# Performance work log

Measured on AMD Instinct MI355X. Metric: run time of the kernel, lower is better.

The kernel has to match this reference:

```python
import jax, jax.numpy as jnp
import numpy as np

SUB_NO = 5
T_NO = 201
H_NO = 64
T_DATA = 50000
E_SYN = 2000
I_SYN = 200


def setup_inputs() -> dict:
    key = jax.random.key(0)
    ks = jax.random.split(key, 10)
    k_conv = 1.0 / np.sqrt(2 * T_NO)   # pytorch Conv1d init bound: 1/sqrt(in_ch/groups * k)
    k_ff = 1.0 / np.sqrt(H_NO)
    k_root = 1.0 / np.sqrt(SUB_NO)
    return {
        "S_e": jax.random.uniform(ks[0], (T_DATA, E_SYN), dtype=jnp.float32),
        "S_i": jax.random.uniform(ks[1], (T_DATA, I_SYN), dtype=jnp.float32),
        "temp": jnp.ones((), dtype=jnp.float32),
        "C_syn_e_raw": jnp.ones((SUB_NO, E_SYN), dtype=jnp.float32),
        "C_syn_i_raw": jnp.ones((SUB_NO, I_SYN), dtype=jnp.float32),
        "conv_w": jax.random.uniform(ks[2], (H_NO * SUB_NO, 2, T_NO), jnp.float32, -k_conv, k_conv),
        "conv_b": jax.random.uniform(ks[3], (H_NO * SUB_NO,), jnp.float32, -k_conv, k_conv),
        "ff_w": jax.random.uniform(ks[4], (SUB_NO, H_NO), jnp.float32, -k_ff, k_ff),
        "ff_b": jax.random.uniform(ks[5], (SUB_NO,), jnp.float32, -k_ff, k_ff),
        "root_w": jax.random.uniform(ks[6], (SUB_NO,), jnp.float32, -k_root, k_root),
        "root_b": jax.random.uniform(ks[7], (), jnp.float32, -k_root, k_root),
        "V_o": jax.random.normal(ks[8], (1,), dtype=jnp.float32),
    }


def reference(S_e, S_i, temp, C_syn_e_raw, C_syn_i_raw, conv_w, conv_b,
              ff_w, ff_b, root_w, root_b, V_o):
    T_data = S_e.shape[0]
    # softmax over subunit axis (axis 0) of the synapse->subunit assignment logits
    C_syn_e = jax.nn.softmax(C_syn_e_raw / temp, axis=0)  # (sub, E)
    C_syn_i = jax.nn.softmax(C_syn_i_raw / temp, axis=0)  # (sub, I)
    S_e_group = S_e @ C_syn_e.T  # (T, sub)
    S_i_group = S_i @ C_syn_i.T  # (T, sub)
    # interleave: channel 2s = excit, 2s+1 = inhib  -> (T, 2*sub)
    S = jnp.stack([S_e_group, S_i_group], axis=2).reshape(T_data, 2 * SUB_NO)
    S = S.T[None]  # (1, 2*sub, T)
    conv_out = jax.lax.conv_general_dilated(
        S, conv_w,
        window_strides=(1,),
        padding=[(T_NO // 2, T_NO // 2)],
        feature_group_count=SUB_NO,
        dimension_numbers=("NCH", "OIH", "NCH"),
    ) + conv_b[None, :, None]          # (1, sub*H, T)
    conv_out = conv_out[0].reshape(SUB_NO, H_NO, T_data)  # (sub, H, T)
    # per-subunit Linear(H,1) + LeakyReLU, fused as an einsum
    sub_out = jnp.einsum("sht,sh->ts", conv_out, ff_w) + ff_b  # (T, sub)
    sub_out = jax.nn.leaky_relu(sub_out, 0.01)
    root_out = jax.nn.leaky_relu(sub_out @ root_w + root_b, 0.01) + V_o[0]  # (T,)
    return root_out
```

## Files before the change

### kernel.cpp

```cpp
#include <hip/hip_runtime.h>
#include <math.h>

#define SUB 5
#define TNO 201
#define HNO 64
#define TDATA 50000
#define ESYN 2000
#define ISYN 200
#define PAD (TNO/2)

#define QE (ESYN/4)
#define QI (ISYN/4)
#define CP 21
#define LDSC ((QE+QI)*CP)

__global__ void weff_kernel(const float* __restrict__ conv_w,
                            const float* __restrict__ conv_b,
                            const float* __restrict__ ff_w,
                            const float* __restrict__ ff_b,
                            float* __restrict__ Weff,
                            float* __restrict__ beff) {
    int idx = blockIdx.x * blockDim.x + threadIdx.x;
    if (idx < SUB * 2 * TNO) {
        int s   = idx / (2 * TNO);
        int rem = idx - s * (2 * TNO);
        float acc = 0.f;
        #pragma unroll 8
        for (int h = 0; h < HNO; ++h)
            acc = fmaf(ff_w[s * HNO + h], conv_w[(size_t)(s * HNO + h) * (2 * TNO) + rem], acc);
        Weff[idx] = acc;
    }
    if (idx < SUB) {
        float acc = ff_b[idx];
        for (int h = 0; h < HNO; ++h)
            acc = fmaf(ff_w[idx * HNO + h], conv_b[idx * HNO + h], acc);
        beff[idx] = acc;
    }
}

__device__ inline float elemf(float4 v, int e) {
    switch (e) { case 0: return v.x; case 1: return v.y; case 2: return v.z; default: return v.w; }
}

__device__ inline float foldp(float a, float b, int m, int lane) {
    float send = (lane & m) ? a : b;
    float recv = __shfl_xor(send, m);
    return ((lane & m) ? b : a) + recv;
}

template<int CH0>
__device__ inline void fma_block(float (&acc)[4][10],
                                 float4 v0, float4 v1, float4 v2, float4 v3,
                                 const float* c) {
    #pragma unroll
    for (int e = 0; e < 4; ++e) {
        float a0 = elemf(v0, e), a1 = elemf(v1, e), a2 = elemf(v2, e), a3 = elemf(v3, e);
        #pragma unroll
        for (int s = 0; s < 5; ++s) {
            float w = c[e * 5 + s];
            acc[0][2 * s + CH0] = fmaf(a0, w, acc[0][2 * s + CH0]);
            acc[1][2 * s + CH0] = fmaf(a1, w, acc[1][2 * s + CH0]);
            acc[2][2 * s + CH0] = fmaf(a2, w, acc[2][2 * s + CH0]);
            acc[3][2 * s + CH0] = fmaf(a3, w, acc[3][2 * s + CH0]);
        }
    }
}

__global__ __launch_bounds__(256) void group_kernel(
        const float* __restrict__ Se, const float* __restrict__ Si,
        const float* __restrict__ rawE, const float* __restrict__ rawI,
        const float* __restrict__ temp,
        float* __restrict__ Sg) {
    __shared__ float ldsC[LDSC];

    float invT = 1.0f / temp[0];
    for (int j = threadIdx.x; j < ESYN + ISYN; j += blockDim.x) {
        float v[SUB];
        float* dst;
        if (j < ESYN) {
            #pragma unroll
            for (int s = 0; s < SUB; ++s) v[s] = rawE[s * ESYN + j] * invT;
            dst = ldsC + (j >> 2) * CP + (j & 3) * SUB;
        } else {
            int jj = j - ESYN;
            #pragma unroll
            for (int s = 0; s < SUB; ++s) v[s] = rawI[s * ISYN + jj] * invT;
            dst = ldsC + QE * CP + (jj >> 2) * CP + (jj & 3) * SUB;
        }
        float m = fmaxf(fmaxf(fmaxf(v[0], v[1]), fmaxf(v[2], v[3])), v[4]);
        float sum = 0.f;
        #pragma unroll
        for (int s = 0; s < SUB; ++s) { v[s] = expf(v[s] - m); sum += v[s]; }
        float r = 1.0f / sum;
        #pragma unroll
        for (int s = 0; s < SUB; ++s) dst[s] = v[s] * r;
    }
    __syncthreads();

    const float* lE = ldsC;
    const float* lI = ldsC + QE * CP;
    int wave = threadIdx.x >> 6;
    int lane = threadIdx.x & 63;
    int nw   = (gridDim.x * blockDim.x) >> 6;
    int wid  = blockIdx.x * (blockDim.x >> 6) + wave;

    for (int g = wid; g < TDATA / 4; g += nw) {
        int t0 = g * 4;
        float acc[4][10];
        #pragma unroll
        for (int r = 0; r < 4; ++r)
            #pragma unroll
            for (int c = 0; c < 10; ++c) acc[r][c] = 0.f;

        const float4* R0 = (const float4*)(Se + (size_t)(t0 + 0) * ESYN);
        const float4* R1 = (const float4*)(Se + (size_t)(t0 + 1) * ESYN);
        const float4* R2 = (const float4*)(Se + (size_t)(t0 + 2) * ESYN);
        const float4* R3 = (const float4*)(Se + (size_t)(t0 + 3) * ESYN);

        for (int it = 0; it < 7; ++it) {
            int q = lane + (it << 6);
            float4 v0 = R0[q], v1 = R1[q], v2 = R2[q], v3 = R3[q];
            fma_block<0>(acc, v0, v1, v2, v3, lE + q * CP);
        }
        {
            int q = lane + 448;
            float4 z = make_float4(0.f, 0.f, 0.f, 0.f);
            float4 v0 = z, v1 = z, v2 = z, v3 = z;
            if (q < QE) { v0 = R0[q]; v1 = R1[q]; v2 = R2[q]; v3 = R3[q]; }
            int qc = (q < QE) ? q : 0;
            fma_block<0>(acc, v0, v1, v2, v3, lE + qc * CP);
        }
        if (lane < QI) {
            const float4* I0 = (const float4*)(Si + (size_t)(t0 + 0) * ISYN);
            const float4* I1 = (const float4*)(Si + (size_t)(t0 + 1) * ISYN);
            const float4* I2 = (const float4*)(Si + (size_t)(t0 + 2) * ISYN);
            const float4* I3 = (const float4*)(Si + (size_t)(t0 + 3) * ISYN);
            float4 v0 = I0[lane], v1 = I1[lane], v2 = I2[lane], v3 = I3[lane];
            fma_block<1>(acc, v0, v1, v2, v3, lI + lane * CP);
        }

        float f1[20], f2[10], f3[5];
        {
            const float* a = &acc[0][0];
            #pragma unroll
            for (int j = 0; j < 20; ++j) f1[j] = foldp(a[2 * j], a[2 * j + 1], 1, lane);
            #pragma unroll
            for (int j = 0; j < 10; ++j) f2[j] = foldp(f1[2 * j], f1[2 * j + 1], 2, lane);
            #pragma unroll
            for (int j = 0; j < 5; ++j)  f3[j] = foldp(f2[2 * j], f2[2 * j + 1], 4, lane);
            #pragma unroll
            for (int j = 0; j < 5; ++j) {
                f3[j] += __shfl_xor(f3[j], 8);
                f3[j] += __shfl_xor(f3[j], 16);
                f3[j] += __shfl_xor(f3[j], 32);
            }
        }
        if (lane < 8) {
            #pragma unroll
            for (int j = 0; j < 5; ++j) {
                int i = 8 * j + lane;
                int r = i / 10, c = i - 10 * r;
                Sg[(size_t)(t0 + r) * 10 + c] = f3[j];
            }
        }
    }
}

#define OB 128
#define ORS (OB + TNO - 1)

__global__ __launch_bounds__(128) void out_kernel(
        const float* __restrict__ Sg, const float* __restrict__ Weff,
        const float* __restrict__ beff, const float* __restrict__ root_w,
        const float* __restrict__ root_b, const float* __restrict__ V_o,
        float* __restrict__ out) {
    __shared__ float sS[ORS * 10];

    int tid = threadIdx.x;
    int t0  = blockIdx.x * OB;

    for (int i = tid; i < ORS * 5; i += OB) {
        int rr = i / 5, p = i - rr * 5;
        int rg = t0 - PAD + rr;
        float2 val = make_float2(0.f, 0.f);
        if (rg >= 0 && rg < TDATA) val = *(const float2*)(Sg + (size_t)rg * 10 + p * 2);
        *(float2*)(sS + rr * 10 + p * 2) = val;
    }
    __syncthreads();

    int t = t0 + tid;
    if (t >= TDATA) return;

    float acc[SUB];
    #pragma unroll
    for (int s = 0; s < SUB; ++s) acc[s] = beff[s];

    for (int k = 0; k < TNO; ++k) {
        const float* r = sS + (tid + k) * 10;
        #pragma unroll
        for (int s = 0; s < SUB; ++s) {
            float2 ei = *(const float2*)(r + 2 * s);
            acc[s] = fmaf(ei.x, Weff[s * 402 + k],
                     fmaf(ei.y, Weff[s * 402 + 201 + k], acc[s]));
        }
    }
    auto lk = [](float x) { return x > 0.f ? x : 0.01f * x; };
    float root = root_b[0];
    #pragma unroll
    for (int s = 0; s < SUB; ++s) root += lk(acc[s]) * root_w[s];
    out[t] = lk(root) + V_o[0];
}

extern "C" void kernel_launch(void* const* d_in, const int* in_sizes, int n_in,
                              void* d_out, int out_size, void* d_ws, size_t ws_size,
                              hipStream_t stream) {
    (void)in_sizes; (void)n_in; (void)out_size; (void)ws_size;
    const float* Se     = (const float*)d_in[0];
    const float* Si     = (const float*)d_in[1];
    const float* temp   = (const float*)d_in[2];
    const float* rawE   = (const float*)d_in[3];
    const float* rawI   = (const float*)d_in[4];
    const float* conv_w = (const float*)d_in[5];
    const float* conv_b = (const float*)d_in[6];
    const float* ff_w   = (const float*)d_in[7];
    const float* ff_b   = (const float*)d_in[8];
    const float* root_w = (const float*)d_in[9];
    const float* root_b = (const float*)d_in[10];
    const float* V_o    = (const float*)d_in[11];
    float* out = (float*)d_out;

    float* ws   = (float*)d_ws;
    float* Weff = ws;
    float* beff = ws + 2016;
    float* Sg   = ws + 2048;

    hipLaunchKernelGGL(weff_kernel, dim3(8), dim3(256), 0, stream,
                       conv_w, conv_b, ff_w, ff_b, Weff, beff);
    hipLaunchKernelGGL(group_kernel, dim3(768), dim3(256), 0, stream,
                       Se, Si, rawE, rawI, temp, Sg);
    hipLaunchKernelGGL(out_kernel, dim3((TDATA + OB - 1) / OB), dim3(128), 0, stream,
                       Sg, Weff, beff, root_w, root_b, V_o, out);
}
```

Baseline: 612.5 us.

## Software-pipeline Se loads with nontemporal prefetch and re-layout out_kernel LDS

Restructures the group kernel's row-tile loop so the next chunk of Se (and the first chunk of the next group) is loaded nontemporally while the current chunk is multiplied, and hoists the Si loads ahead of the FMA work. It also raises the launch-bounds occupancy hint to 3 blocks per CU. In out_kernel, the shared-memory staging is transposed to a per-subunit planar layout with padded pitch, and the tap loop gets partial unrolling, aiming to cut LDS bank conflicts. The prefetching raises register pressure, which may conflict with the occupancy target.

After: 716.0 us. +16.9%, slower.

```diff
diff --git a/kernel.cpp b/kernel.cpp
--- a/kernel.cpp
+++ b/kernel.cpp
@@ -13,6 +13,9 @@
 #define QI (ISYN/4)
 #define CP 21
 #define LDSC ((QE+QI)*CP)
+#define NGRP (TDATA/4)
+
+typedef float fx4 __attribute__((ext_vector_type(4)));
 
 __global__ void weff_kernel(const float* __restrict__ conv_w,
                             const float* __restrict__ conv_b,
@@ -38,10 +41,6 @@
     }
 }
 
-__device__ inline float elemf(float4 v, int e) {
-    switch (e) { case 0: return v.x; case 1: return v.y; case 2: return v.z; default: return v.w; }
-}
-
 __device__ inline float foldp(float a, float b, int m, int lane) {
     float send = (lane & m) ? a : b;
     float recv = __shfl_xor(send, m);
@@ -50,23 +49,22 @@
 
 template<int CH0>
 __device__ inline void fma_block(float (&acc)[4][10],
-                                 float4 v0, float4 v1, float4 v2, float4 v3,
+                                 fx4 v0, fx4 v1, fx4 v2, fx4 v3,
                                  const float* c) {
     #pragma unroll
     for (int e = 0; e < 4; ++e) {
-        float a0 = elemf(v0, e), a1 = elemf(v1, e), a2 = elemf(v2, e), a3 = elemf(v3, e);
         #pragma unroll
         for (int s = 0; s < 5; ++s) {
             float w = c[e * 5 + s];
-            acc[0][2 * s + CH0] = fmaf(a0, w, acc[0][2 * s + CH0]);
-            acc[1][2 * s + CH0] = fmaf(a1, w, acc[1][2 * s + CH0]);
-            acc[2][2 * s + CH0] = fmaf(a2, w, acc[2][2 * s + CH0]);
-            acc[3][2 * s + CH0] = fmaf(a3, w, acc[3][2 * s + CH0]);
-        }
-    }
-}
-
-__global__ __launch_bounds__(256) void group_kernel(
+            acc[0][2 * s + CH0] = fmaf(v0[e], w, acc[0][2 * s + CH0]);
+            acc[1][2 * s + CH0] = fmaf(v1[e], w, acc[1][2 * s + CH0]);
+            acc[2][2 * s + CH0] = fmaf(v2[e], w, acc[2][2 * s + CH0]);
+            acc[3][2 * s + CH0] = fmaf(v3[e], w, acc[3][2 * s + CH0]);
+        }
+    }
+}
+
+__global__ __launch_bounds__(256, 3) void group_kernel(
         const float* __restrict__ Se, const float* __restrict__ Si,
         const float* __restrict__ rawE, const float* __restrict__ rawI,
         const float* __restrict__ temp,
@@ -104,40 +102,70 @@
     int nw   = (gridDim.x * blockDim.x) >> 6;
     int wid  = blockIdx.x * (blockDim.x >> 6) + wave;
 
-    for (int g = wid; g < TDATA / 4; g += nw) {
-        int t0 = g * 4;
+    const fx4* SeV = (const fx4*)Se;
+    const fx4* SiV = (const fx4*)Si;
+
+    fx4 c0, c1, c2, c3;
+    {
+        size_t b = (size_t)wid * 4 * QE;
+        c0 = __builtin_nontemporal_load(SeV + b + 0 * QE + lane);
+        c1 = __builtin_nontemporal_load(SeV + b + 1 * QE + lane);
+        c2 = __builtin_nontemporal_load(SeV + b + 2 * QE + lane);
+        c3 = __builtin_nontemporal_load(SeV + b + 3 * QE + lane);
+    }
+
+    for (int g = wid; g < NGRP; g += nw) {
+        size_t bE = (size_t)g * 4 * QE;
+
+        fx4 i0, i1, i2, i3;
+        {
+            int li = (lane < QI) ? lane : 0;
+            size_t bI = (size_t)g * 4 * QI;
+            i0 = __builtin_nontemporal_load(SiV + bI + 0 * QI + li);
+            i1 = __builtin_nontemporal_load(SiV + bI + 1 * QI + li);
+            i2 = __builtin_nontemporal_load(SiV + bI + 2 * QI + li);
+            i3 = __builtin_nontemporal_load(SiV + bI + 3 * QI + li);
+        }
+
         float acc[4][10];
         #pragma unroll
         for (int r = 0; r < 4; ++r)
             #pragma unroll
             for (int c = 0; c < 10; ++c) acc[r][c] = 0.f;
 
-        const float4* R0 = (const float4*)(Se + (size_t)(t0 + 0) * ESYN);
-        const float4* R1 = (const float4*)(Se + (size_t)(t0 + 1) * ESYN);
-        const float4* R2 = (const float4*)(Se + (size_t)(t0 + 2) * ESYN);
-        const float4* R3 = (const float4*)(Se + (size_t)(t0 + 3) * ESYN);
-
-        for (int it = 0; it < 7; ++it) {
+        int gn = g + nw;
+        size_t bN = (size_t)((gn < NGRP) ? gn : wid) * 4 * QE;
+
+        #pragma unroll
+        for (int it = 0; it < 8; ++it) {
+            fx4 n0, n1, n2, n3;
+            if (it < 7) {
+                int qn = lane + ((it + 1) << 6);
+                int qc = (qn < QE) ? qn : 0;
+                n0 = __builtin_nontemporal_load(SeV + bE + 0 * QE + qc);
+                n1 = __builtin_nontemporal_load(SeV + bE + 1 * QE + qc);
+                n2 = __builtin_nontemporal_load(SeV + bE + 2 * QE + qc);
+                n3 = __builtin_nontemporal_load(SeV + bE + 3 * QE + qc);
+            } else {
+                n0 = __builtin_nontemporal_load(SeV + bN + 0 * QE + lane);
+                n1 = __builtin_nontemporal_load(SeV + bN + 1 * QE + lane);
+                n2 = __builtin_nontemporal_load(SeV + bN + 2 * QE + lane);
+                n3 = __builtin_nontemporal_load(SeV + bN + 3 * QE + lane);
+            }
             int q = lane + (it << 6);
-            float4 v0 = R0[q], v1 = R1[q], v2 = R2[q], v3 = R3[q];
-            fma_block<0>(acc, v0, v1, v2, v3, lE + q * CP);
-        }
-        {
-            int q = lane + 448;
-            float4 z = make_float4(0.f, 0.f, 0.f, 0.f);
-            float4 v0 = z, v1 = z, v2 = z, v3 = z;
-            if (q < QE) { v0 = R0[q]; v1 = R1[q]; v2 = R2[q]; v3 = R3[q]; }
-            int qc = (q < QE) ? q : 0;
-            fma_block<0>(acc, v0, v1, v2, v3, lE + qc * CP);
-        }
-        if (lane < QI) {
-            const float4* I0 = (const float4*)(Si + (size_t)(t0 + 0) * ISYN);
-            const float4* I1 = (const float4*)(Si + (size_t)(t0 + 1) * ISYN);
-            const float4* I2 = (const float4*)(Si + (size_t)(t0 + 2) * ISYN);
-            const float4* I3 = (const float4*)(Si + (size_t)(t0 + 3) * ISYN);
-            float4 v0 = I0[lane], v1 = I1[lane], v2 = I2[lane], v3 = I3[lane];
-            fma_block<1>(acc, v0, v1, v2, v3, lI + lane * CP);
-        }
+            if (it == 7) {
+                bool ok = (q < QE);
+                fx4 z = (fx4)0.f;
+                if (!ok) { c0 = z; c1 = z; c2 = z; c3 = z; }
+                int qc = ok ? q : 0;
+                fma_block<0>(acc, c0, c1, c2, c3, lE + qc * CP);
+            } else {
+                fma_block<0>(acc, c0, c1, c2, c3, lE + q * CP);
+            }
+            c0 = n0; c1 = n1; c2 = n2; c3 = n3;
+        }
+
+        if (lane < QI) fma_block<1>(acc, i0, i1, i2, i3, lI + lane * CP);
 
         float f1[20], f2[10], f3[5];
         {
@@ -160,7 +188,7 @@
             for (int j = 0; j < 5; ++j) {
                 int i = 8 * j + lane;
                 int r = i / 10, c = i - 10 * r;
-                Sg[(size_t)(t0 + r) * 10 + c] = f3[j];
+                Sg[(size_t)(g * 4 + r) * 10 + c] = f3[j];
             }
         }
     }
@@ -168,23 +196,24 @@
 
 #define OB 128
 #define ORS (OB + TNO - 1)
+#define PPITCH (ORS * 2 + 2)
 
 __global__ __launch_bounds__(128) void out_kernel(
         const float* __restrict__ Sg, const float* __restrict__ Weff,
         const float* __restrict__ beff, const float* __restrict__ root_w,
         const float* __restrict__ root_b, const float* __restrict__ V_o,
         float* __restrict__ out) {
-    __shared__ float sS[ORS * 10];
+    __shared__ float sP[SUB * PPITCH];
 
     int tid = threadIdx.x;
     int t0  = blockIdx.x * OB;
 
-    for (int i = tid; i < ORS * 5; i += OB) {
-        int rr = i / 5, p = i - rr * 5;
+    for (int i = tid; i < ORS * SUB; i += OB) {
+        int rr = i % ORS, s = i / ORS;
         int rg = t0 - PAD + rr;
         float2 val = make_float2(0.f, 0.f);
-        if (rg >= 0 && rg < TDATA) val = *(const float2*)(Sg + (size_t)rg * 10 + p * 2);
-        *(float2*)(sS + rr * 10 + p * 2) = val;
+        if (rg >= 0 && rg < TDATA) val = *(const float2*)(Sg + (size_t)rg * 10 + s * 2);
+        *(float2*)(sP + s * PPITCH + rr * 2) = val;
     }
     __syncthreads();
 
@@ -195,11 +224,12 @@
     #pragma unroll
     for (int s = 0; s < SUB; ++s) acc[s] = beff[s];
 
+    #pragma unroll 3
     for (int k = 0; k < TNO; ++k) {
-        const float* r = sS + (tid + k) * 10;
+        int r2 = (tid + k) * 2;
         #pragma unroll
         for (int s = 0; s < SUB; ++s) {
-            float2 ei = *(const float2*)(r + 2 * s);
+            float2 ei = *(const float2*)(sP + s * PPITCH + r2);
             acc[s] = fmaf(ei.x, Weff[s * 402 + k],
                      fmaf(ei.y, Weff[s * 402 + 201 + k], acc[s]));
         }
```
